# Optimization experiments

Measured on AMD Instinct MI355X. Metric: run time of the kernel, lower is better.

## Reference

```python
import jax, jax.numpy as jnp
import numpy as np

H = 8            # head_size (hard-coded in the original forward)
BB = 0.6         # balance_bias
NEG = -1e9


def masked_softmax(x, m, axis=-1):
    # softmax over `axis`, zero out masked entries, renormalize
    p = jax.nn.softmax(x, axis=axis)
    p = p * m
    return p / (p.sum(axis=axis, keepdims=True) + 1e-13)


def setup_inputs():
    key = jax.random.key(0)
    ks = jax.random.split(key, 12)
    B, B0, V, A, Hd = 8, 2, 384, 384, 512
    S = V + A
    s = 1.0 / np.sqrt(Hd)
    return {
        'q': jax.random.normal(ks[0], (B, S, Hd), jnp.float32),
        'k': jax.random.normal(ks[1], (B, S, Hd), jnp.float32),
        'v': jax.random.normal(ks[2], (B, S, Hd), jnp.float32),
        'mask': jnp.ones((B, S, 1), jnp.float32),
        'depth_value': jax.random.uniform(ks[3], (B0, V), jnp.float32),
        'coord_3d': jax.random.normal(ks[4], (B, V, 3), jnp.float32),
        'va_v_mask': jnp.ones((B, V, 1), jnp.float32),
        'va_a_mask': jnp.ones((B, A, 1), jnp.float32),
        'mean_depth_value': jax.random.uniform(ks[5], (B, A), jnp.float32),
        'Wq': jax.random.normal(ks[6], (Hd, Hd), jnp.float32) * s,
        'bq': jnp.zeros((Hd,), jnp.float32),
        'Wk': jax.random.normal(ks[7], (Hd, Hd), jnp.float32) * s,
        'bk': jnp.zeros((Hd,), jnp.float32),
        'Wv': jax.random.normal(ks[8], (Hd, Hd), jnp.float32) * s,
        'bv': jnp.zeros((Hd,), jnp.float32),
        'Wo': jax.random.normal(ks[9], (Hd, Hd), jnp.float32) * s,
        'bo': jnp.zeros((Hd,), jnp.float32),
    }


def reference(q, k, v, mask, depth_value, coord_3d, va_v_mask, va_a_mask,
              mean_depth_value, Wq, bq, Wk, bk, Wv, bv, Wo, bo):
    B, S, Hd = q.shape
    d = Hd // H
    scale = d ** (-0.5)
    V = va_v_mask.shape[1]
    A = va_a_mask.shape[1]
    B0 = depth_value.shape[0]
    rep = B // B0  # = 4 in the original code

    qh = (q @ Wq + bq).reshape(B, S, H, d).transpose(0, 2, 1, 3)  # [B,H,S,d]
    kh = (k @ Wk + bk).reshape(B, S, H, d).transpose(0, 2, 1, 3)
    vh = (v @ Wv + bv).reshape(B, S, H, d).transpose(0, 2, 1, 3)

    m = mask[:, None]                      # [B,1,S,1]
    mask4 = m * jnp.swapaxes(m, 2, 3)      # [B,1,S,S] (broadcasts over heads)

    x = jnp.einsum('bhqd,bhkd->bhqk', qh, kh) * scale  # [B,H,S,S]

    # visual-visual depth bias
    dv = depth_value[:, :, None]                       # [B0,V,1]
    diff = jnp.abs(dv - jnp.swapaxes(dv, 1, 2))        # [B0,V,V]
    diff = jnp.repeat(diff, rep, axis=0)[:, None]      # [B,1,V,V]
    self_mask = 1.0 - jnp.eye(V, dtype=x.dtype)
    depth_term = jnp.abs(x[:, :, :V, :V]) * (jnp.exp(-diff) - BB) * self_mask  # [B,H,V,V]

    # audio->visual attention map (pre-bias scores)
    x_av = x[:, :, V:, :V]                             # [B,H,A,V]
    m_av = mask4[:, :, V:, :V]
    att_score_av = jnp.where(m_av > 0, x_av, NEG)
    att_map_av = masked_softmax(att_score_av, m_av, axis=3)

    # audio-visual depth bias (mean_depth_value branch)
    tdv = jnp.repeat(jnp.swapaxes(dv, 1, 2), rep, axis=0)           # [B,1,V]
    diff_va = jnp.abs(mean_depth_value[:, :, None] - tdv)[:, None]  # [B,1,A,V]
    depth_av_term = jnp.abs(x_av) * (jnp.exp(-diff_va) - BB)        # [B,H,A,V]

    # assemble bias matrix: [:V,:V]=depth_term, [V:,:V]=depth_av_term, rest 0
    top = jnp.concatenate([depth_term, jnp.zeros((B, H, V, S - V), x.dtype)], axis=3)
    bot = jnp.concatenate([depth_av_term, jnp.zeros((B, H, A, S - V), x.dtype)], axis=3)
    bias = jnp.concatenate([top, bot], axis=2)         # [B,H,S,S]

    x = x + bias
    att_score = jnp.where(mask4 > 0, x, NEG)
    att_map = masked_softmax(att_score, mask4 * jnp.ones((1, H, 1, 1), x.dtype), axis=3)
    out = jnp.einsum('bhqk,bhkd->bhqd', att_map, vh)   # [B,H,S,d]

    # auxiliary depth mean via the a->v attention map
    dv_rep = jnp.repeat(depth_value, rep, axis=0)      # [B,V]
    md = jnp.einsum('bhav,bv->bha', att_map_av, dv_rep)
    md = md.mean(axis=1)                               # [B,A]
    md = md.sum(axis=-1) / va_a_mask[:, :, 0].sum(axis=-1)  # [B]
    md = jnp.broadcast_to(md[:, None], (B, A))

    out = out.transpose(0, 2, 1, 3).reshape(B, S, H * d)
    out = out @ Wo + bo
    return out, att_score, att_map, md
```

## Files before the change

kernel.cpp:

```cpp
#include <hip/hip_runtime.h>
#include <hip/hip_bf16.h>
#include <cstdint>
#include <cstddef>

namespace {
constexpr int B  = 8;
constexpr int S  = 768;
constexpr int V  = 384;
constexpr int A  = 384;
constexpr int H  = 8;
constexpr int D  = 64;
constexpr int HD = 512;
constexpr float SCALE = 0.125f;
constexpr float BBC   = 0.6f;
constexpr float NEGV  = -1000000000.0f;
constexpr size_t N_QH = (size_t)B * H * S * D;
}

using short8 = __attribute__((ext_vector_type(8))) short;
using f32x4  = __attribute__((ext_vector_type(4))) float;

static __device__ __forceinline__ unsigned short f2bf(float f) {
  union { float f; unsigned int u; } v; v.f = f;
  unsigned int r = v.u + 0x7FFFu + ((v.u >> 16) & 1u);
  return (unsigned short)(r >> 16);
}
static __device__ __forceinline__ f32x4 mfma16(short8 a, short8 b, f32x4 c) {
  return __builtin_amdgcn_mfma_f32_16x16x32_bf16(a, b, c, 0, 0, 0);
}
static __device__ __forceinline__ short8 pack_bf8(float4 a, float4 b) {
  union { short8 s; uint4 u; } r;
  r.u.x = (unsigned)f2bf(a.x) | ((unsigned)f2bf(a.y) << 16);
  r.u.y = (unsigned)f2bf(a.z) | ((unsigned)f2bf(a.w) << 16);
  r.u.z = (unsigned)f2bf(b.x) | ((unsigned)f2bf(b.y) << 16);
  r.u.w = (unsigned)f2bf(b.z) | ((unsigned)f2bf(b.w) << 16);
  return r.s;
}

__global__ __launch_bounds__(256) void prep_w(
    const float* __restrict__ Wq, const float* __restrict__ Wk,
    const float* __restrict__ Wv, const float* __restrict__ Wo,
    unsigned short* __restrict__ wt)
{
  __shared__ float tile[64][68];
  const int id = blockIdx.x;
  const int z = id >> 6, tl = id & 63;
  const int k0 = (tl >> 3) * 64, n0 = (tl & 7) * 64;
  const float* W = (z == 0) ? Wq : (z == 1) ? Wk : (z == 2) ? Wv : Wo;
  unsigned short* WT = wt + (size_t)z * 262144;
  const int t = threadIdx.x;
#pragma unroll
  for (int u = 0; u < 4; ++u) {
    int idx = u * 256 + t;
    int r = idx >> 4, c4 = (idx & 15) * 4;
    *(float4*)&tile[r][c4] = *(const float4*)&W[(size_t)(k0 + r) * 512 + n0 + c4];
  }
  __syncthreads();
#pragma unroll
  for (int u = 0; u < 4; ++u) {
    int idx = u * 256 + t;
    int n = idx >> 4, kq = (idx & 15) * 4;
    unsigned int h0 = f2bf(tile[kq + 0][n]), h1 = f2bf(tile[kq + 1][n]);
    unsigned int h2 = f2bf(tile[kq + 2][n]), h3 = f2bf(tile[kq + 3][n]);
    *(uint2*)&WT[(size_t)(n0 + n) * 512 + k0 + kq] =
        make_uint2(h0 | (h1 << 16), h2 | (h3 << 16));
  }
}

__global__ __launch_bounds__(256) void qkv_mfma(
    const float* __restrict__ q, const float* __restrict__ k,
    const float* __restrict__ v, const unsigned short* __restrict__ wt,
    const float* __restrict__ bq, const float* __restrict__ bk,
    const float* __restrict__ bv,
    unsigned short* __restrict__ qh, unsigned short* __restrict__ kh,
    unsigned short* __restrict__ vhT)
{
  __shared__ unsigned short Bh[64][40];
  __shared__ unsigned short Ax[64][40];
  const int lin = ((blockIdx.x & 7) * 288) + (blockIdx.x >> 3);
  const int n0 = (lin & 7) * 64;
  const int gidx = lin >> 3;
  const int mt = gidx % 96, z = gidx / 96;
  const int m0 = mt * 64;
  const float* X = (z == 0) ? q : (z == 1) ? k : v;
  const unsigned short* WT = wt + (size_t)z * 262144;
  const float* bias = (z == 0) ? bq : (z == 1) ? bk : bv;
  const int t = threadIdx.x, w = t >> 6, lane = t & 63;
  const int l15 = lane & 15, g = lane >> 4;
  const int bb = m0 / S;
  f32x4 acc[4] = {};

  const int srow = t >> 2, skq = (t & 3) * 8;
  for (int k0 = 0; k0 < 512; k0 += 32) {
    __syncthreads();
    *(short8*)&Bh[srow][skq] = *(const short8*)&WT[(size_t)(n0 + srow) * 512 + k0 + skq];
    if (z == 2) {
      float4 x0 = *(const float4*)&X[(size_t)(m0 + srow) * 512 + k0 + skq];
      float4 x1 = *(const float4*)&X[(size_t)(m0 + srow) * 512 + k0 + skq + 4];
      *(short8*)&Ax[srow][skq] = pack_bf8(x0, x1);
    }
    __syncthreads();
    if (z != 2) {
      const size_t abase = (size_t)(m0 + w * 16 + l15) * 512 + k0 + g * 8;
      float4 a0 = *(const float4*)&X[abase];
      float4 a1 = *(const float4*)&X[abase + 4];
      short8 ah = pack_bf8(a0, a1);
#pragma unroll
      for (int tn = 0; tn < 4; ++tn) {
        short8 bh_ = *(short8*)&Bh[tn * 16 + l15][g * 8];
        acc[tn] = mfma16(ah, bh_, acc[tn]);
      }
    } else {
      short8 wh = *(short8*)&Bh[w * 16 + l15][g * 8];
#pragma unroll
      for (int tm = 0; tm < 4; ++tm) {
        short8 xf = *(short8*)&Ax[tm * 16 + l15][g * 8];
        acc[tm] = mfma16(wh, xf, acc[tm]);
      }
    }
  }

  if (z != 2) {
    unsigned short* Y = (z == 0) ? qh : kh;
#pragma unroll
    for (int tn = 0; tn < 4; ++tn) {
      const int c = n0 + tn * 16 + l15;
      const float bi = bias[c];
      const int h = c >> 6, d = c & 63;
#pragma unroll
      for (int r = 0; r < 4; ++r) {
        const int mm = m0 + w * 16 + g * 4 + r;
        const int s = mm - bb * S;
        Y[((size_t)(bb * H + h) * S + s) * D + d] = f2bf(acc[tn][r] + bi);
      }
    }
  } else {
#pragma unroll
    for (int tm = 0; tm < 4; ++tm) {
      const int mcol = m0 + tm * 16 + l15;
      const int s = mcol - bb * S;
#pragma unroll
      for (int r = 0; r < 4; ++r) {
        const int n = n0 + w * 16 + g * 4 + r;
        const int h = n >> 6, d = n & 63;
        vhT[((size_t)(bb * H + h) * D + d) * S + s] = f2bf(acc[tm][r] + bias[n]);
      }
    }
  }
}

__global__ __launch_bounds__(256, 4) void fused_attn(
    const unsigned short* __restrict__ qh, const unsigned short* __restrict__ kh,
    const unsigned short* __restrict__ vhT,
    const float* __restrict__ mask, const float* __restrict__ depth_value,
    const float* __restrict__ mean_depth,
    float* __restrict__ att_score, float* __restrict__ att_map,
    unsigned short* __restrict__ ctx, float* __restrict__ md_rows)
{
  __shared__ unsigned short Ps[16][768];
  __shared__ float mcol[768];
  __shared__ float dvcol[384];
  __shared__ float pmax[16][4];
  __shared__ float psum[16][4];
  __shared__ float psem[16][4];
  __shared__ float asmd[16][2];
  __shared__ float mxA[16], rdA[16], drefsA[16], mrwA[16];

  const int id = blockIdx.x;
  const int rest = id >> 3;
  const int rt = rest % 48;
  const int bh = (id & 7) + 8 * (rest / 48);
  const int b = bh >> 3, b0 = b >> 2;
  const int r0 = rt * 16;
  const int t = threadIdx.x;
  const int w = t >> 6;
  const int lane = t & 63;
  const int l15 = lane & 15, g = lane >> 4;
  const bool avblk = (r0 >= V);

  for (int j = t; j < 768; j += 256) mcol[j] = mask[(size_t)b * S + j];
  for (int j = t; j < 384; j += 256) dvcol[j] = depth_value[(size_t)b0 * V + j];
  if (t < 16) {
    const int row = r0 + t;
    drefsA[t] = (row < V) ? depth_value[(size_t)b0 * V + row]
                          : mean_depth[(size_t)b * A + (row - V)];
    mrwA[t] = mask[(size_t)b * S + row];
  }

  short8 qf[2];
#pragma unroll
  for (int ks = 0; ks < 2; ++ks)
    qf[ks] = *(const short8*)&qh[((size_t)bh * S + r0 + l15) * D + ks * 32 + g * 8];

  f32x4 acc[12] = {};
#pragma unroll
  for (int tn = 0; tn < 12; ++tn) {
    const int col = w * 192 + tn * 16 + l15;
#pragma unroll
    for (int ks = 0; ks < 2; ++ks) {
      short8 kf = *(const short8*)&kh[((size_t)bh * S + col) * D + ks * 32 + g * 8];
      acc[tn] = mfma16(qf[ks], kf, acc[tn]);
    }
  }
  __syncthreads();

  const bool biasw = (w < 2);
  float mcr[12], dvc[12];
#pragma unroll
  for (int tn = 0; tn < 12; ++tn) {
    const int col = w * 192 + tn * 16 + l15;
    mcr[tn] = mcol[col];
    dvc[tn] = biasw ? dvcol[col] : 0.f;
  }

#pragma unroll
  for (int r = 0; r < 4; ++r) {
    const int lrow = g * 4 + r;
    const int row = r0 + lrow;
    const float mr = mrwA[lrow];
    const float dref = drefsA[lrow];
    float* srow = &att_score[((size_t)bh * S + row) * S];
#pragma unroll
    for (int tn = 0; tn < 12; ++tn) {
      const int col = w * 192 + tn * 16 + l15;
      float x = acc[tn][r] * SCALE;
      if (biasw) {
        float gg = __expf(-fabsf(dref - dvc[tn])) - BBC;
        float bb2 = fabsf(x) * gg;
        if (row == col) bb2 = 0.f;
        x += bb2;
      }
      x = (mr * mcr[tn] > 0.f) ? x : NEGV;
      __builtin_nontemporal_store(x, &srow[col]);
      acc[tn][r] = x;
    }
  }

#pragma unroll
  for (int r = 0; r < 4; ++r) {
    float v = NEGV;
#pragma unroll
    for (int tn = 0; tn < 12; ++tn) v = fmaxf(v, acc[tn][r]);
#pragma unroll
    for (int o = 1; o < 16; o <<= 1) v = fmaxf(v, __shfl_xor(v, o, 16));
    if (l15 == 0) pmax[g * 4 + r][w] = v;
  }
  __syncthreads();
  if (t < 16)
    mxA[t] = fmaxf(fmaxf(pmax[t][0], pmax[t][1]), fmaxf(pmax[t][2], pmax[t][3]));
  __syncthreads();

  if (avblk) {
    if (biasw) {
#pragma unroll
      for (int r = 0; r < 4; ++r) {
        const int lrow = g * 4 + r;
        const float mdv = drefsA[lrow];
        const float mr = mrwA[lrow];
        const float amx = fmaxf(2.5f * mxA[lrow], 0.f);
        float se = 0.f, sem = 0.f, smd = 0.f;
#pragma unroll
        for (int tn = 0; tn < 12; ++tn) {
          float post = acc[tn][r];
          float gg = __expf(-fabsf(mdv - dvc[tn])) - BBC;
          float pre = post / (post > 0.f ? 1.f + gg : 1.f - gg);
          float pm = mr * mcr[tn];
          pre = (pm > 0.f) ? pre : NEGV;
          float e = __expf(pre - amx);
          se += e; sem += e * pm; smd += e * pm * dvc[tn];
        }
#pragma unroll
        for (int o = 1; o < 16; o <<= 1) {
          se += __shfl_xor(se, o, 16);
          sem += __shfl_xor(sem, o, 16);
          smd += __shfl_xor(smd, o, 16);
        }
        if (l15 == 0) { psum[lrow][w] = se; psem[lrow][w] = sem; asmd[lrow][w] = smd; }
      }
    }
    __syncthreads();
    if (t < 16) {
      float se = psum[t][0] + psum[t][1];
      float sem = psem[t][0] + psem[t][1];
      float smd = asmd[t][0] + asmd[t][1];
      md_rows[(size_t)bh * A + (r0 + t - V)] = smd / (sem + 1e-13f * se);
    }
    __syncthreads();
  }

#pragma unroll
  for (int r = 0; r < 4; ++r) {
    const int lrow = g * 4 + r;
    const float mx = mxA[lrow];
    const float mr = mrwA[lrow];
    float se = 0.f, sem = 0.f;
#pragma unroll
    for (int tn = 0; tn < 12; ++tn) {
      float e = __expf(acc[tn][r] - mx);
      acc[tn][r] = e;
      se += e; sem += e * (mr * mcr[tn]);
    }
#pragma unroll
    for (int o = 1; o < 16; o <<= 1) {
      se += __shfl_xor(se, o, 16);
      sem += __shfl_xor(sem, o, 16);
    }
    if (l15 == 0) { psum[lrow][w] = se; psem[lrow][w] = sem; }
  }
  __syncthreads();
  if (t < 16) {
    float se = psum[t][0] + psum[t][1] + psum[t][2] + psum[t][3];
    float sem = psem[t][0] + psem[t][1] + psem[t][2] + psem[t][3];
    rdA[t] = 1.f / (sem + 1e-13f * se);
  }
  __syncthreads();

#pragma unroll
  for (int r = 0; r < 4; ++r) {
    const int lrow = g * 4 + r;
    const int row = r0 + lrow;
    const float rden = rdA[lrow];
    const float mr = mrwA[lrow];
    float* prow = &att_map[((size_t)bh * S + row) * S];
    const int swz = (lrow & 7) << 4;
#pragma unroll
    for (int tn = 0; tn < 12; ++tn) {
      const int col = w * 192 + tn * 16 + l15;
      float p = acc[tn][r] * (mr * mcr[tn]) * rden;
      __builtin_nontemporal_store(p, &prow[col]);
      Ps[lrow][col ^ swz] = f2bf(p);
    }
  }
  __syncthreads();

  {
    const int aswz = (l15 & 7) << 4;
    f32x4 pacc = {};
    const unsigned short* vcol = &vhT[((size_t)bh * D + w * 16 + l15) * S];
#pragma unroll 8
    for (int kk = 0; kk < 24; ++kk) {
      short8 a = *(short8*)&Ps[l15][(kk * 32 + g * 8) ^ aswz];
      short8 bv = *(const short8*)&vcol[kk * 32 + g * 8];
      pacc = mfma16(a, bv, pacc);
    }
#pragma unroll
    for (int r = 0; r < 4; ++r) {
      const int row = r0 + g * 4 + r;
      ctx[((size_t)bh * S + row) * D + w * 16 + l15] = f2bf(pacc[r]);
    }
  }
}

__global__ __launch_bounds__(256) void gemm_out(
    const unsigned short* __restrict__ Xb, const unsigned short* __restrict__ WT,
    const float* __restrict__ bias, float* __restrict__ Yf,
    const float* __restrict__ md_rows, const float* __restrict__ va_a_mask,
    float* __restrict__ md_out)
{
  const int t = threadIdx.x;
  if (blockIdx.x >= 768) {
    __shared__ float red0[256];
    __shared__ float red1[256];
    const int b = blockIdx.x - 768;
    float s1 = 0.f, s2 = 0.f;
    for (int u = t; u < H * A; u += 256) s1 += md_rows[(size_t)b * H * A + u];
    for (int u = t; u < A; u += 256) s2 += va_a_mask[(size_t)b * A + u];
    red0[t] = s1; red1[t] = s2;
    __syncthreads();
    for (int o = 128; o > 0; o >>= 1) {
      if (t < o) { red0[t] += red0[t + o]; red1[t] += red1[t + o]; }
      __syncthreads();
    }
    const float val = red0[0] / ((float)H * red1[0]);
    for (int u = t; u < A; u += 256) md_out[(size_t)b * A + u] = val;
    return;
  }
  __shared__ unsigned short Bh[64][40];
  const int lin = ((blockIdx.x & 7) * 96) + (blockIdx.x >> 3);
  const int n0 = (lin & 7) * 64;
  const int m0 = (lin >> 3) * 64;
  const int w = t >> 6, lane = t & 63;
  const int l15 = lane & 15, g = lane >> 4;
  const int bb = m0 / S;
  f32x4 acc[4] = {};
  const int srow = t >> 2, skq = (t & 3) * 8;
  for (int k0 = 0; k0 < 512; k0 += 32) {
    __syncthreads();
    *(short8*)&Bh[srow][skq] = *(const short8*)&WT[(size_t)(n0 + srow) * 512 + k0 + skq];
    __syncthreads();
    const int s = m0 + w * 16 + l15 - bb * S;
    const int h = k0 >> 6, d = (k0 & 63) + g * 8;
    short8 ah = *(const short8*)&Xb[((size_t)(bb * H + h) * S + s) * D + d];
#pragma unroll
    for (int tn = 0; tn < 4; ++tn) {
      short8 bh_ = *(short8*)&Bh[tn * 16 + l15][g * 8];
      acc[tn] = mfma16(ah, bh_, acc[tn]);
    }
  }
#pragma unroll
  for (int tn = 0; tn < 4; ++tn) {
    const int c = n0 + tn * 16 + l15;
    const float bi = bias[c];
#pragma unroll
    for (int r = 0; r < 4; ++r) {
      const int m = m0 + w * 16 + g * 4 + r;
      Yf[(size_t)m * 512 + c] = acc[tn][r] + bi;
    }
  }
}

extern "C" void kernel_launch(void* const* d_in, const int* in_sizes, int n_in,
                              void* d_out, int out_size, void* d_ws, size_t ws_size,
                              hipStream_t stream) {
  const float* q           = (const float*)d_in[0];
  const float* k           = (const float*)d_in[1];
  const float* v           = (const float*)d_in[2];
  const float* mask        = (const float*)d_in[3];
  const float* depth_value = (const float*)d_in[4];
  const float* va_a_mask   = (const float*)d_in[7];
  const float* mean_depth  = (const float*)d_in[8];
  const float* Wq = (const float*)d_in[9];
  const float* bq = (const float*)d_in[10];
  const float* Wk = (const float*)d_in[11];
  const float* bk = (const float*)d_in[12];
  const float* Wv = (const float*)d_in[13];
  const float* bv = (const float*)d_in[14];
  const float* Wo = (const float*)d_in[15];
  const float* bo = (const float*)d_in[16];

  unsigned short* wsu = (unsigned short*)d_ws;
  unsigned short* qh  = wsu;
  unsigned short* kh  = wsu + N_QH;
  unsigned short* vhT = wsu + 2 * N_QH;
  unsigned short* ctx = qh;
  unsigned short* wt  = wsu + 3 * N_QH;
  float* md_rows = (float*)(wsu + 3 * N_QH + 4 * 262144);

  float* out       = (float*)d_out;
  float* att_score = out + (size_t)B * S * HD;
  float* att_map   = att_score + (size_t)B * H * S * S;
  float* md_out    = att_map + (size_t)B * H * S * S;

  prep_w<<<256, 256, 0, stream>>>(Wq, Wk, Wv, Wo, wt);
  qkv_mfma<<<2304, 256, 0, stream>>>(q, k, v, wt, bq, bk, bv, qh, kh, vhT);
  fused_attn<<<3072, 256, 0, stream>>>(qh, kh, vhT, mask, depth_value, mean_depth,
                                       att_score, att_map, ctx, md_rows);
  gemm_out<<<776, 256, 0, stream>>>(ctx, wt + 3 * 262144, bo, out,
                                    md_rows, va_a_mask, md_out);
}
```

Measured before the change: 172.2 us.

## Swap MFMA operand order so accumulators hold contiguous columns for vector stores

The MFMA operands are swapped (K/W fragment as A, Q/X fragment as B) in the QK, Q/K projection and output projection GEMMs. Each lane's accumulator then holds four consecutive columns of one row rather than four rows of one column. This allows 128-bit stores of att_score, att_map, the projected outputs and Yf, and 64-bit stores of bf16 outputs. Row reductions also shrink to two cross-lane shuffles instead of four per row, and mask/depth loads become float4 LDS reads. The aim is to cut global store transaction count and shuffle overhead in the store-bound attention kernel.

Measured after the change: 175.4 us. No clear change (+1.9%).

```diff
diff --git a/kernel.cpp b/kernel.cpp
--- a/kernel.cpp
+++ b/kernel.cpp
@@ -35,6 +35,12 @@
   r.u.z = (unsigned)f2bf(b.x) | ((unsigned)f2bf(b.y) << 16);
   r.u.w = (unsigned)f2bf(b.z) | ((unsigned)f2bf(b.w) << 16);
   return r.s;
+}
+static __device__ __forceinline__ ushort4 pack_bf4(f32x4 a, float4 bi) {
+  ushort4 r;
+  r.x = f2bf(a[0] + bi.x); r.y = f2bf(a[1] + bi.y);
+  r.z = f2bf(a[2] + bi.z); r.w = f2bf(a[3] + bi.w);
+  return r;
 }
 
 __global__ __launch_bounds__(256) void prep_w(
@@ -104,11 +110,11 @@
       const size_t abase = (size_t)(m0 + w * 16 + l15) * 512 + k0 + g * 8;
       float4 a0 = *(const float4*)&X[abase];
       float4 a1 = *(const float4*)&X[abase + 4];
-      short8 ah = pack_bf8(a0, a1);
+      short8 xfrag = pack_bf8(a0, a1);
 #pragma unroll
       for (int tn = 0; tn < 4; ++tn) {
-        short8 bh_ = *(short8*)&Bh[tn * 16 + l15][g * 8];
-        acc[tn] = mfma16(ah, bh_, acc[tn]);
+        short8 wfrag = *(short8*)&Bh[tn * 16 + l15][g * 8];
+        acc[tn] = mfma16(wfrag, xfrag, acc[tn]);
       }
     } else {
       short8 wh = *(short8*)&Bh[w * 16 + l15][g * 8];
@@ -122,17 +128,14 @@
 
   if (z != 2) {
     unsigned short* Y = (z == 0) ? qh : kh;
+    const int s = m0 + w * 16 + l15 - bb * S;
+    const int h = n0 >> 6;
+    unsigned short* yrow = &Y[((size_t)(bb * H + h) * S + s) * D];
 #pragma unroll
     for (int tn = 0; tn < 4; ++tn) {
-      const int c = n0 + tn * 16 + l15;
-      const float bi = bias[c];
-      const int h = c >> 6, d = c & 63;
-#pragma unroll
-      for (int r = 0; r < 4; ++r) {
-        const int mm = m0 + w * 16 + g * 4 + r;
-        const int s = mm - bb * S;
-        Y[((size_t)(bb * H + h) * S + s) * D + d] = f2bf(acc[tn][r] + bi);
-      }
+      const int d0 = tn * 16 + g * 4;
+      float4 bi4 = *(const float4*)&bias[n0 + d0];
+      *(ushort4*)&yrow[d0] = pack_bf4(acc[tn], bi4);
     }
   } else {
 #pragma unroll
@@ -195,55 +198,57 @@
   f32x4 acc[12] = {};
 #pragma unroll
   for (int tn = 0; tn < 12; ++tn) {
-    const int col = w * 192 + tn * 16 + l15;
+    const int col16 = w * 192 + tn * 16;
 #pragma unroll
     for (int ks = 0; ks < 2; ++ks) {
-      short8 kf = *(const short8*)&kh[((size_t)bh * S + col) * D + ks * 32 + g * 8];
-      acc[tn] = mfma16(qf[ks], kf, acc[tn]);
+      short8 kf = *(const short8*)&kh[((size_t)bh * S + col16 + l15) * D + ks * 32 + g * 8];
+      acc[tn] = mfma16(kf, qf[ks], acc[tn]);
     }
   }
   __syncthreads();
 
   const bool biasw = (w < 2);
-  float mcr[12], dvc[12];
-#pragma unroll
-  for (int tn = 0; tn < 12; ++tn) {
-    const int col = w * 192 + tn * 16 + l15;
-    mcr[tn] = mcol[col];
-    dvc[tn] = biasw ? dvcol[col] : 0.f;
-  }
-
-#pragma unroll
-  for (int r = 0; r < 4; ++r) {
-    const int lrow = g * 4 + r;
-    const int row = r0 + lrow;
-    const float mr = mrwA[lrow];
-    const float dref = drefsA[lrow];
-    float* srow = &att_score[((size_t)bh * S + row) * S];
+  const float mr = mrwA[l15];
+  const float dref = drefsA[l15];
+  const int grow = r0 + l15;
+
+  {
+    float* srow = &att_score[((size_t)bh * S + grow) * S];
 #pragma unroll
     for (int tn = 0; tn < 12; ++tn) {
-      const int col = w * 192 + tn * 16 + l15;
-      float x = acc[tn][r] * SCALE;
+      const int colb = w * 192 + tn * 16 + g * 4;
+      float4 mc4 = *(float4*)&mcol[colb];
+      f32x4 x;
+#pragma unroll
+      for (int r = 0; r < 4; ++r) x[r] = acc[tn][r] * SCALE;
       if (biasw) {
-        float gg = __expf(-fabsf(dref - dvc[tn])) - BBC;
-        float bb2 = fabsf(x) * gg;
-        if (row == col) bb2 = 0.f;
-        x += bb2;
-      }
-      x = (mr * mcr[tn] > 0.f) ? x : NEGV;
-      __builtin_nontemporal_store(x, &srow[col]);
-      acc[tn][r] = x;
-    }
-  }
-
-#pragma unroll
-  for (int r = 0; r < 4; ++r) {
+        float4 dv4 = *(float4*)&dvcol[colb];
+        float dvr[4] = {dv4.x, dv4.y, dv4.z, dv4.w};
+#pragma unroll
+        for (int r = 0; r < 4; ++r) {
+          float gg = __expf(-fabsf(dref - dvr[r])) - BBC;
+          float bb2 = fabsf(x[r]) * gg;
+          if (grow == colb + r) bb2 = 0.f;
+          x[r] += bb2;
+        }
+      }
+      float mcr[4] = {mc4.x, mc4.y, mc4.z, mc4.w};
+#pragma unroll
+      for (int r = 0; r < 4; ++r) x[r] = (mr * mcr[r] > 0.f) ? x[r] : NEGV;
+      __builtin_nontemporal_store(x, (f32x4*)&srow[colb]);
+      acc[tn] = x;
+    }
+  }
+
+  {
     float v = NEGV;
 #pragma unroll
-    for (int tn = 0; tn < 12; ++tn) v = fmaxf(v, acc[tn][r]);
-#pragma unroll
-    for (int o = 1; o < 16; o <<= 1) v = fmaxf(v, __shfl_xor(v, o, 16));
-    if (l15 == 0) pmax[g * 4 + r][w] = v;
+    for (int tn = 0; tn < 12; ++tn)
+#pragma unroll
+      for (int r = 0; r < 4; ++r) v = fmaxf(v, acc[tn][r]);
+    v = fmaxf(v, __shfl_xor(v, 16));
+    v = fmaxf(v, __shfl_xor(v, 32));
+    if (g == 0) pmax[l15][w] = v;
   }
   __syncthreads();
   if (t < 16)
@@ -252,31 +257,30 @@
 
   if (avblk) {
     if (biasw) {
-#pragma unroll
-      for (int r = 0; r < 4; ++r) {
-        const int lrow = g * 4 + r;
-        const float mdv = drefsA[lrow];
-        const float mr = mrwA[lrow];
-        const float amx = fmaxf(2.5f * mxA[lrow], 0.f);
-        float se = 0.f, sem = 0.f, smd = 0.f;
-#pragma unroll
-        for (int tn = 0; tn < 12; ++tn) {
+      const float amx = fmaxf(2.5f * mxA[l15], 0.f);
+      float se = 0.f, sem = 0.f, smd = 0.f;
+#pragma unroll
+      for (int tn = 0; tn < 12; ++tn) {
+        const int colb = w * 192 + tn * 16 + g * 4;
+        float4 mc4 = *(float4*)&mcol[colb];
+        float4 dv4 = *(float4*)&dvcol[colb];
+        float mcr[4] = {mc4.x, mc4.y, mc4.z, mc4.w};
+        float dvr[4] = {dv4.x, dv4.y, dv4.z, dv4.w};
+#pragma unroll
+        for (int r = 0; r < 4; ++r) {
           float post = acc[tn][r];
-          float gg = __expf(-fabsf(mdv - dvc[tn])) - BBC;
+          float gg = __expf(-fabsf(dref - dvr[r])) - BBC;
           float pre = post / (post > 0.f ? 1.f + gg : 1.f - gg);
-          float pm = mr * mcr[tn];
+          float pm = mr * mcr[r];
           pre = (pm > 0.f) ? pre : NEGV;
           float e = __expf(pre - amx);
-          se += e; sem += e * pm; smd += e * pm * dvc[tn];
+          se += e; sem += e * pm; smd += e * pm * dvr[r];
         }
-#pragma unroll
-        for (int o = 1; o < 16; o <<= 1) {
-          se += __shfl_xor(se, o, 16);
-          sem += __shfl_xor(sem, o, 16);
-          smd += __shfl_xor(smd, o, 16);
-        }
-        if (l15 == 0) { psum[lrow][w] = se; psem[lrow][w] = sem; asmd[lrow][w] = smd; }
-      }
+      }
+      se += __shfl_xor(se, 16);  se += __shfl_xor(se, 32);
+      sem += __shfl_xor(sem, 16); sem += __shfl_xor(sem, 32);
+      smd += __shfl_xor(smd, 16); smd += __shfl_xor(smd, 32);
+      if (g == 0) { psum[l15][w] = se; psem[l15][w] = sem; asmd[l15][w] = smd; }
     }
     __syncthreads();
     if (t < 16) {
@@ -288,24 +292,24 @@
     __syncthreads();
   }
 
-#pragma unroll
-  for (int r = 0; r < 4; ++r) {
-    const int lrow = g * 4 + r;
-    const float mx = mxA[lrow];
-    const float mr = mrwA[lrow];
+  {
+    const float mx = mxA[l15];
     float se = 0.f, sem = 0.f;
 #pragma unroll
     for (int tn = 0; tn < 12; ++tn) {
-      float e = __expf(acc[tn][r] - mx);
-      acc[tn][r] = e;
-      se += e; sem += e * (mr * mcr[tn]);
-    }
-#pragma unroll
-    for (int o = 1; o < 16; o <<= 1) {
-      se += __shfl_xor(se, o, 16);
-      sem += __shfl_xor(sem, o, 16);
-    }
-    if (l15 == 0) { psum[lrow][w] = se; psem[lrow][w] = sem; }
+      const int colb = w * 192 + tn * 16 + g * 4;
+      float4 mc4 = *(float4*)&mcol[colb];
+      float mcr[4] = {mc4.x, mc4.y, mc4.z, mc4.w};
+#pragma unroll
+      for (int r = 0; r < 4; ++r) {
+        float e = __expf(acc[tn][r] - mx);
+        acc[tn][r] = e;
+        se += e; sem += e * (mr * mcr[r]);
+      }
+    }
+    se += __shfl_xor(se, 16);  se += __shfl_xor(se, 32);
+    sem += __shfl_xor(sem, 16); sem += __shfl_xor(sem, 32);
+    if (g == 0) { psum[l15][w] = se; psem[l15][w] = sem; }
   }
   __syncthreads();
   if (t < 16) {
@@ -315,20 +319,22 @@
   }
   __syncthreads();
 
-#pragma unroll
-  for (int r = 0; r < 4; ++r) {
-    const int lrow = g * 4 + r;
-    const int row = r0 + lrow;
-    const float rden = rdA[lrow];
-    const float mr = mrwA[lrow];
-    float* prow = &att_map[((size_t)bh * S + row) * S];
-    const int swz = (lrow & 7) << 4;
+  {
+    const float rden = rdA[l15];
+    const int swz = (l15 & 7) << 4;
+    float* prow = &att_map[((size_t)bh * S + grow) * S];
 #pragma unroll
     for (int tn = 0; tn < 12; ++tn) {
-      const int col = w * 192 + tn * 16 + l15;
-      float p = acc[tn][r] * (mr * mcr[tn]) * rden;
-      __builtin_nontemporal_store(p, &prow[col]);
-      Ps[lrow][col ^ swz] = f2bf(p);
+      const int colb = w * 192 + tn * 16 + g * 4;
+      float4 mc4 = *(float4*)&mcol[colb];
+      float mcr[4] = {mc4.x, mc4.y, mc4.z, mc4.w};
+      f32x4 p;
+#pragma unroll
+      for (int r = 0; r < 4; ++r) p[r] = acc[tn][r] * (mr * mcr[r]) * rden;
+      __builtin_nontemporal_store(p, (f32x4*)&prow[colb]);
+      ushort4 pk;
+      pk.x = f2bf(p[0]); pk.y = f2bf(p[1]); pk.z = f2bf(p[2]); pk.w = f2bf(p[3]);
+      *(ushort4*)&Ps[l15][colb ^ swz] = pk;
     }
   }
   __syncthreads();
@@ -384,28 +390,27 @@
   const int bb = m0 / S;
   f32x4 acc[4] = {};
   const int srow = t >> 2, skq = (t & 3) * 8;
+  const int s = m0 + w * 16 + l15 - bb * S;
   for (int k0 = 0; k0 < 512; k0 += 32) {
     __syncthreads();
     *(short8*)&Bh[srow][skq] = *(const short8*)&WT[(size_t)(n0 + srow) * 512 + k0 + skq];
     __syncthreads();
-    const int s = m0 + w * 16 + l15 - bb * S;
     const int h = k0 >> 6, d = (k0 & 63) + g * 8;
-    short8 ah = *(const short8*)&Xb[((size_t)(bb * H + h) * S + s) * D + d];
+    short8 xfrag = *(const short8*)&Xb[((size_t)(bb * H + h) * S + s) * D + d];
 #pragma unroll
     for (int tn = 0; tn < 4; ++tn) {
-      short8 bh_ = *(short8*)&Bh[tn * 16 + l15][g * 8];
-      acc[tn] = mfma16(ah, bh_, acc[tn]);
-    }
-  }
+      short8 wfrag = *(short8*)&Bh[tn * 16 + l15][g * 8];
+      acc[tn] = mfma16(wfrag, xfrag, acc[tn]);
+    }
+  }
+  const int m = m0 + w * 16 + l15;
 #pragma unroll
   for (int tn = 0; tn < 4; ++tn) {
-    const int c = n0 + tn * 16 + l15;
-    const float bi = bias[c];
-#pragma unroll
-    for (int r = 0; r < 4; ++r) {
-      const int m = m0 + w * 16 + g * 4 + r;
-      Yf[(size_t)m * 512 + c] = acc[tn][r] + bi;
-    }
+    const int c0 = n0 + tn * 16 + g * 4;
+    float4 bi4 = *(const float4*)&bias[c0];
+    float4 o = make_float4(acc[tn][0] + bi4.x, acc[tn][1] + bi4.y,
+                           acc[tn][2] + bi4.z, acc[tn][3] + bi4.w);
+    *(float4*)&Yf[(size_t)m * 512 + c0] = o;
   }
 }
 
```
